# Kernel optimization log

Measured on AMD Instinct MI355X. Metric: run time of the kernel, lower is better.

## Reference

```python
import jax, jax.numpy as jnp
import numpy as np

NEG_SLOPE = 0.01  # torch nn.LeakyReLU default


def setup_inputs() -> dict:
    key = jax.random.key(0)
    k1, k2 = jax.random.split(key)
    B, L, N = 32, 512, 1024
    X = jax.random.normal(k1, (B, L, N), dtype=jnp.float32)
    W = jax.random.normal(k2, (1, 2 * L), dtype=jnp.float32) * (1.0 / np.sqrt(2 * L))
    return {"X": X, "W": W}


def reference(X, W):
    # X: [B, L, N]; W: [1, 2L] weight of Linear(2L, 1, bias=False)
    L = X.shape[1]
    N = X.shape[2]
    w1 = W[0, :L]   # applied to X[:, :, i]
    w2 = W[0, L:]   # applied to X[:, :, j]
    s1 = jnp.einsum('bln,l->bn', X, w1)  # [B, N]
    s2 = jnp.einsum('bln,l->bn', X, w2)  # [B, N]
    # e[b,i,j] = leaky_relu(s1[b,i] + s2[b,j]) for i != j, 0 on the diagonal
    e = jax.nn.leaky_relu(s1[:, :, None] + s2[:, None, :], NEG_SLOPE)  # [B, N, N]
    diag = jnp.eye(N, dtype=bool)
    e = jnp.where(diag[None, :, :], 0.0, e)
    # softmax over dim=1 (over i), matching torch.softmax(e, dim=1)
    alpha = jax.nn.softmax(e, axis=1)  # [B, N, N]
    # h = bmm(alpha, X^T)^T: h[b,l,i] = sum_j alpha[b,i,j] * X[b,l,j]
    h = jnp.einsum('bij,blj->bli', alpha, X)  # [B, L, N]
    return jax.nn.sigmoid(h)
```

## Files before the change

kernel.cpp:

```cpp
#include <hip/hip_runtime.h>
#include <hip/hip_bf16.h>

#define BATCH 32
#define LSEQ  512
#define NDIM  1024
#define NSPLIT 16

typedef __attribute__((ext_vector_type(8))) short bf16x8;
typedef __attribute__((ext_vector_type(4))) float f32x4;

__device__ __forceinline__ unsigned short f2bf(float x) {
    __hip_bfloat16 h = __float2bfloat16(x);
    return __builtin_bit_cast(unsigned short, h);
}

__global__ __launch_bounds__(256) void prep_kernel(
    const float* __restrict__ X, const float* __restrict__ W,
    unsigned short* __restrict__ Xb, float* __restrict__ P1, float* __restrict__ P2)
{
    __shared__ float sw[2 * LSEQ];
    int tid = threadIdx.x;
    for (int i = tid; i < 2 * LSEQ; i += 256) sw[i] = W[i];
    __syncthreads();

    int b  = blockIdx.y;
    int sp = blockIdx.x;
    int l0 = sp * (LSEQ / NSPLIT);
    size_t base = ((size_t)b * LSEQ + l0) * NDIM + tid * 4;
    const float* xp = X + base;
    unsigned short* xbp = Xb + base;

    float a0=0,a1=0,a2=0,a3=0, c0=0,c1=0,c2=0,c3=0;
    for (int l = 0; l < LSEQ / NSPLIT; ++l) {
        float4 x = *(const float4*)(xp + (size_t)l * NDIM);
        float w1 = sw[l0 + l], w2 = sw[LSEQ + l0 + l];
        a0 = fmaf(x.x, w1, a0); a1 = fmaf(x.y, w1, a1);
        a2 = fmaf(x.z, w1, a2); a3 = fmaf(x.w, w1, a3);
        c0 = fmaf(x.x, w2, c0); c1 = fmaf(x.y, w2, c1);
        c2 = fmaf(x.z, w2, c2); c3 = fmaf(x.w, w2, c3);
        ushort4 u; u.x = f2bf(x.x); u.y = f2bf(x.y); u.z = f2bf(x.z); u.w = f2bf(x.w);
        *(ushort4*)(xbp + (size_t)l * NDIM) = u;
    }
    size_t po = ((size_t)sp * BATCH + b) * NDIM + tid * 4;
    *(float4*)(P1 + po) = make_float4(a0, a1, a2, a3);
    *(float4*)(P2 + po) = make_float4(c0, c1, c2, c3);
}

__global__ __launch_bounds__(256) void stats_kernel(
    const float* __restrict__ P1, const float* __restrict__ P2,
    float* __restrict__ s1, float* __restrict__ s2, float* __restrict__ rd)
{
    __shared__ float s1s[NDIM];
    __shared__ float s2s[128];
    int t = threadIdx.x;
    int b = blockIdx.x >> 3, sl = blockIdx.x & 7;
    int j0 = sl * 128;

    #pragma unroll
    for (int q = 0; q < 4; ++q) {
        int n = q * 256 + t;
        float a = 0.f;
        #pragma unroll
        for (int sp = 0; sp < NSPLIT; ++sp)
            a += P1[((size_t)sp * BATCH + b) * NDIM + n];
        s1s[n] = a;
        if (sl == 0) s1[b * NDIM + n] = a;
    }
    if (t < 128) {
        int j = j0 + t;
        float c = 0.f;
        #pragma unroll
        for (int sp = 0; sp < NSPLIT; ++sp)
            c += P2[((size_t)sp * BATCH + b) * NDIM + j];
        s2s[t] = c;
        s2[b * NDIM + j] = c;
    }
    __syncthreads();

    int jl = t >> 1, half = t & 1;
    int jg = j0 + jl;
    float s2j = s2s[jl];
    float sum = 0.f;
    int i0 = half * 512;
    for (int i = i0; i < i0 + 512; ++i) {
        float v = s1s[i] + s2j;
        v = fmaxf(v, 0.01f * v);
        if (i == jg) v = 0.f;
        sum += __expf(v);
    }
    sum += __shfl_xor(sum, 1);
    if (half == 0) rd[b * NDIM + jg] = 1.0f / sum;
}

__global__ __launch_bounds__(256) void btgen_kernel(
    const float* __restrict__ s1, const float* __restrict__ s2,
    const float* __restrict__ rd, unsigned short* __restrict__ Bt)
{
    int wid = threadIdx.x >> 6, lane = threadIdx.x & 63;
    int r = blockIdx.x * 4 + wid;
    int b = r >> 10, i = r & 1023;
    float s1i = s1[r];
    const float* s2b = s2 + b * NDIM;
    const float* rdb = rd + b * NDIM;
    unsigned short* outp = Bt + (size_t)r * NDIM;

    #pragma unroll
    for (int q = 0; q < 2; ++q) {
        int j0 = q * 512 + lane * 8;
        float sv[8], rv[8];
        #pragma unroll
        for (int h = 0; h < 2; ++h) {
            float4 s4 = *(const float4*)(s2b + j0 + h * 4);
            float4 r4 = *(const float4*)(rdb + j0 + h * 4);
            sv[h*4+0]=s4.x; sv[h*4+1]=s4.y; sv[h*4+2]=s4.z; sv[h*4+3]=s4.w;
            rv[h*4+0]=r4.x; rv[h*4+1]=r4.y; rv[h*4+2]=r4.z; rv[h*4+3]=r4.w;
        }
        bf16x8 v;
        #pragma unroll
        for (int k = 0; k < 8; ++k) {
            float e = s1i + sv[k];
            e = fmaxf(e, 0.01f * e);
            if (j0 + k == i) e = 0.f;
            v[k] = (short)f2bf(__expf(e) * rv[k]);
        }
        *(bf16x8*)&outp[j0] = v;
    }
}

__global__ __launch_bounds__(256) void gemm_kernel(
    const unsigned short* __restrict__ Xb, const unsigned short* __restrict__ Bt,
    float* __restrict__ out)
{
    __shared__ __align__(16) unsigned short Xs[2 * 128 * 32];
    __shared__ __align__(16) unsigned short Bs[2 * 128 * 32];

    int tid = threadIdx.x, wid = tid >> 6, lane = tid & 63;
    int wm = wid >> 1, wn = wid & 1;

    int flat = blockIdx.x;
    int xcd   = flat & 7;
    int idx   = flat >> 3;
    int bg    = idx >> 5;
    int inner = idx & 31;
    int b  = bg * 8 + xcd;
    int n0 = (inner & 7) * 128;
    int l0 = (inner >> 3) * 128;

    const unsigned short* Xg = Xb + ((size_t)b * LSEQ + l0) * NDIM;
    const unsigned short* Bg = Bt + ((size_t)b * NDIM + n0) * NDIM;

    int rin = lane >> 2, ch = lane & 3;

    f32x4 acc[4][4] = {};

    for (int kb = 0; kb < 16; ++kb) {
        int k0 = kb * 64;
        __syncthreads();
        #pragma unroll
        for (int kh = 0; kh < 2; ++kh) {
            #pragma unroll
            for (int q = 0; q < 2; ++q) {
                int row = wid * 32 + q * 16 + rin;
                int kg = k0 + kh * 32 + ch * 8;
                const unsigned short* gx = Xg + (size_t)row * NDIM + kg;
                const unsigned short* gb = Bg + (size_t)row * NDIM + kg;
                unsigned short* lx = &Xs[kh * 4096 + (wid * 32 + q * 16) * 32];
                unsigned short* lb = &Bs[kh * 4096 + (wid * 32 + q * 16) * 32];
                __builtin_amdgcn_global_load_lds(
                    (const __attribute__((address_space(1))) void*)gx,
                    (__attribute__((address_space(3))) void*)lx, 16, 0, 0);
                __builtin_amdgcn_global_load_lds(
                    (const __attribute__((address_space(1))) void*)gb,
                    (__attribute__((address_space(3))) void*)lb, 16, 0, 0);
            }
        }
        __syncthreads();

        int rsel = lane & 15, ksel = (lane >> 4) * 8;
        #pragma unroll
        for (int kh = 0; kh < 2; ++kh) {
            bf16x8 av[4], bv[4];
            #pragma unroll
            for (int mi = 0; mi < 4; ++mi)
                av[mi] = *(const bf16x8*)&Xs[kh * 4096 + (wm * 64 + mi * 16 + rsel) * 32 + ksel];
            #pragma unroll
            for (int ni = 0; ni < 4; ++ni)
                bv[ni] = *(const bf16x8*)&Bs[kh * 4096 + (wn * 64 + ni * 16 + rsel) * 32 + ksel];
            #pragma unroll
            for (int mi = 0; mi < 4; ++mi)
                #pragma unroll
                for (int ni = 0; ni < 4; ++ni)
                    acc[mi][ni] = __builtin_amdgcn_mfma_f32_16x16x32_bf16(
                        av[mi], bv[ni], acc[mi][ni], 0, 0, 0);
        }
    }

    float* outb = out + ((size_t)b * LSEQ + l0) * NDIM + n0;
    int rq = lane >> 4, cl = lane & 15;
    #pragma unroll
    for (int mi = 0; mi < 4; ++mi)
        #pragma unroll
        for (int ni = 0; ni < 4; ++ni) {
            int col = wn * 64 + ni * 16 + cl;
            #pragma unroll
            for (int r2 = 0; r2 < 4; ++r2) {
                int row = wm * 64 + mi * 16 + rq * 4 + r2;
                float v = acc[mi][ni][r2];
                outb[(size_t)row * NDIM + col] = 1.0f / (1.0f + __expf(-v));
            }
        }
}

extern "C" void kernel_launch(void* const* d_in, const int* in_sizes, int n_in,
                              void* d_out, int out_size, void* d_ws, size_t ws_size,
                              hipStream_t stream) {
    (void)in_sizes; (void)n_in; (void)out_size; (void)ws_size;
    const float* X = (const float*)d_in[0];
    const float* W = (const float*)d_in[1];
    float* out = (float*)d_out;

    float* s1 = (float*)d_ws;
    float* s2 = s1 + BATCH * NDIM;
    float* rd = s2 + BATCH * NDIM;
    float* P1 = rd + BATCH * NDIM;
    float* P2 = P1 + (size_t)NSPLIT * BATCH * NDIM;
    unsigned short* Xb = (unsigned short*)(P2 + (size_t)NSPLIT * BATCH * NDIM);
    unsigned short* Bt = Xb + (size_t)BATCH * LSEQ * NDIM;

    prep_kernel<<<dim3(NSPLIT, BATCH), 256, 0, stream>>>(X, W, Xb, P1, P2);
    stats_kernel<<<256, 256, 0, stream>>>(P1, P2, s1, s2, rd);
    btgen_kernel<<<(BATCH * NDIM) / 4, 256, 0, stream>>>(s1, s2, rd, Bt);
    gemm_kernel<<<1024, 256, 0, stream>>>(Xb, Bt, out);
}
```

Measured before the change: 199.6 us.

## Rewrite GEMM with 256x256 tiles, 4-stage LDS pipeline and swizzled layout

The batched GEMM kernel now uses 512-thread blocks computing 256x256 output tiles, fed by a 4-deep ring of LDS buffers filled with direct global-to-LDS loads and gated by vmcnt waits with one barrier per k-step. LDS rows are XOR-swizzled to avoid bank conflicts, and MFMA issue is wrapped in setprio. The aim is to hide global-load latency and raise data reuse per loaded byte. In exchange each wave holds more accumulators and the block uses 128KB of LDS, and only 256 blocks are launched, which may limit occupancy and load balance across CUs.

```diff
diff --git a/kernel.cpp b/kernel.cpp
--- a/kernel.cpp
+++ b/kernel.cpp
@@ -127,89 +127,111 @@
     }
 }
 
-__global__ __launch_bounds__(256) void gemm_kernel(
+#define WAITVM(n) asm volatile("s_waitcnt vmcnt(" #n ")" ::: "memory")
+#define FENCE()   asm volatile("" ::: "memory")
+
+#define DO_STAGE(bufi) {                                                        \
+    _Pragma("unroll")                                                           \
+    for (int j = 0; j < 4; ++j) {                                               \
+        __builtin_amdgcn_global_load_lds(                                       \
+            (const __attribute__((address_space(1))) void*)srcp[j],             \
+            (__attribute__((address_space(3))) void*)(LdsC + (bufi) * 32768 +   \
+                                                      ldst0 + j * 8192),        \
+            16, 0, 0);                                                          \
+        srcp[j] += 64;                       \
+    } }
+
+#define COMPUTE(bufi) {                                                         \
+    const char* Lb = LdsC + (bufi) * 32768;                                     \
+    bf16x8 av[8]; bf16x8 bv[4];                                                 \
+    _Pragma("unroll")                                                           \
+    for (int mi = 0; mi < 8; ++mi)                                              \
+        av[mi] = *(const bf16x8*)(Lb + abase0 + mi * 2048);                     \
+    _Pragma("unroll")                                                           \
+    for (int ni = 0; ni < 4; ++ni)                                              \
+        bv[ni] = *(const bf16x8*)(Lb + bbase0 + ni * 2048);                     \
+    __builtin_amdgcn_s_setprio(1);                                              \
+    _Pragma("unroll")                                                           \
+    for (int ni = 0; ni < 4; ++ni)                                              \
+        _Pragma("unroll")                                                       \
+        for (int mi = 0; mi < 8; ++mi)                                          \
+            acc[mi][ni] = __builtin_amdgcn_mfma_f32_16x16x32_bf16(              \
+                av[mi], bv[ni], acc[mi][ni], 0, 0, 0);                          \
+    __builtin_amdgcn_s_setprio(0);                                              \
+}
+
+__global__ __launch_bounds__(512, 2) void gemm_kernel(
     const unsigned short* __restrict__ Xb, const unsigned short* __restrict__ Bt,
     float* __restrict__ out)
 {
-    __shared__ __align__(16) unsigned short Xs[2 * 128 * 32];
-    __shared__ __align__(16) unsigned short Bs[2 * 128 * 32];
-
-    int tid = threadIdx.x, wid = tid >> 6, lane = tid & 63;
-    int wm = wid >> 1, wn = wid & 1;
-
-    int flat = blockIdx.x;
+    __shared__ __align__(16) unsigned short LDSU[65536];
+    char* LdsC = (char*)LDSU;
+
+    const int tid = threadIdx.x, lane = tid & 63, wid = tid >> 6;
+    const int wm = wid >> 2, wn = wid & 3;
+
+    int flat  = blockIdx.x;
     int xcd   = flat & 7;
-    int idx   = flat >> 3;
-    int bg    = idx >> 5;
-    int inner = idx & 31;
-    int b  = bg * 8 + xcd;
-    int n0 = (inner & 7) * 128;
-    int l0 = (inner >> 3) * 128;
-
-    const unsigned short* Xg = Xb + ((size_t)b * LSEQ + l0) * NDIM;
-    const unsigned short* Bg = Bt + ((size_t)b * NDIM + n0) * NDIM;
-
-    int rin = lane >> 2, ch = lane & 3;
-
-    f32x4 acc[4][4] = {};
-
-    for (int kb = 0; kb < 16; ++kb) {
-        int k0 = kb * 64;
-        __syncthreads();
-        #pragma unroll
-        for (int kh = 0; kh < 2; ++kh) {
-            #pragma unroll
-            for (int q = 0; q < 2; ++q) {
-                int row = wid * 32 + q * 16 + rin;
-                int kg = k0 + kh * 32 + ch * 8;
-                const unsigned short* gx = Xg + (size_t)row * NDIM + kg;
-                const unsigned short* gb = Bg + (size_t)row * NDIM + kg;
-                unsigned short* lx = &Xs[kh * 4096 + (wid * 32 + q * 16) * 32];
-                unsigned short* lb = &Bs[kh * 4096 + (wid * 32 + q * 16) * 32];
-                __builtin_amdgcn_global_load_lds(
-                    (const __attribute__((address_space(1))) void*)gx,
-                    (__attribute__((address_space(3))) void*)lx, 16, 0, 0);
-                __builtin_amdgcn_global_load_lds(
-                    (const __attribute__((address_space(1))) void*)gb,
-                    (__attribute__((address_space(3))) void*)lb, 16, 0, 0);
-            }
-        }
-        __syncthreads();
-
-        int rsel = lane & 15, ksel = (lane >> 4) * 8;
-        #pragma unroll
-        for (int kh = 0; kh < 2; ++kh) {
-            bf16x8 av[4], bv[4];
-            #pragma unroll
-            for (int mi = 0; mi < 4; ++mi)
-                av[mi] = *(const bf16x8*)&Xs[kh * 4096 + (wm * 64 + mi * 16 + rsel) * 32 + ksel];
-            #pragma unroll
-            for (int ni = 0; ni < 4; ++ni)
-                bv[ni] = *(const bf16x8*)&Bs[kh * 4096 + (wn * 64 + ni * 16 + rsel) * 32 + ksel];
-            #pragma unroll
-            for (int mi = 0; mi < 4; ++mi)
-                #pragma unroll
-                for (int ni = 0; ni < 4; ++ni)
-                    acc[mi][ni] = __builtin_amdgcn_mfma_f32_16x16x32_bf16(
-                        av[mi], bv[ni], acc[mi][ni], 0, 0, 0);
-        }
-    }
+    int p     = flat >> 3;
+    int b     = (p >> 3) * 8 + xcd;
+    int inner = p & 7;
+    int mt = inner & 1, nt = inner >> 1;
+    int l0 = mt * 256, n0 = nt * 256;
+
+    const char* XgB = (const char*)(Xb + ((size_t)b * LSEQ + l0) * NDIM);
+    const char* BgB = (const char*)(Bt + ((size_t)b * NDIM + n0) * NDIM);
+
+    const char* srcp[4];
+    #pragma unroll
+    for (int j = 0; j < 4; ++j) {
+        int c = tid + j * 512;
+        int r = c >> 3, slot = c & 7;
+        int off = (slot * 16) ^ ((r & 7) << 4);
+        srcp[j] = (off < 64) ? XgB + (size_t)r * 2048 + off
+                             : BgB + (size_t)r * 2048 + (off - 64);
+    }
+    const int ldst0 = wid * 1024;
+
+    const int rsel = lane & 15, kq = lane >> 4;
+    const int swz  = (rsel & 7) << 4;
+    const int abase0 = wm * 16384 + rsel * 128 + ((kq * 16) ^ swz);
+    const int bbase0 = wn * 8192  + rsel * 128 + (((64 + kq * 16)) ^ swz);
+
+    f32x4 acc[8][4] = {};
+
+    DO_STAGE(0); DO_STAGE(1); DO_STAGE(2);
+
+    for (int t = 0; t < 29; ++t) {
+        WAITVM(8);
+        __builtin_amdgcn_s_barrier();
+        FENCE();
+        DO_STAGE((t + 3) & 3);
+        COMPUTE(t & 3);
+    }
+    WAITVM(8); __builtin_amdgcn_s_barrier(); FENCE(); COMPUTE(1);
+    WAITVM(4); __builtin_amdgcn_s_barrier(); FENCE(); COMPUTE(2);
+    WAITVM(0); __builtin_amdgcn_s_barrier(); FENCE(); COMPUTE(3);
 
     float* outb = out + ((size_t)b * LSEQ + l0) * NDIM + n0;
-    int rq = lane >> 4, cl = lane & 15;
-    #pragma unroll
-    for (int mi = 0; mi < 4; ++mi)
+    const int rq = lane >> 4, cl = lane & 15;
+    #pragma unroll
+    for (int mi = 0; mi < 8; ++mi)
         #pragma unroll
         for (int ni = 0; ni < 4; ++ni) {
             int col = wn * 64 + ni * 16 + cl;
             #pragma unroll
             for (int r2 = 0; r2 < 4; ++r2) {
-                int row = wm * 64 + mi * 16 + rq * 4 + r2;
+                int row = wm * 128 + mi * 16 + rq * 4 + r2;
                 float v = acc[mi][ni][r2];
                 outb[(size_t)row * NDIM + col] = 1.0f / (1.0f + __expf(-v));
             }
         }
 }
+
+#undef WAITVM
+#undef FENCE
+#undef DO_STAGE
+#undef COMPUTE
 
 extern "C" void kernel_launch(void* const* d_in, const int* in_sizes, int n_in,
                               void* d_out, int out_size, void* d_ws, size_t ws_size,
@@ -230,5 +252,5 @@
     prep_kernel<<<dim3(NSPLIT, BATCH), 256, 0, stream>>>(X, W, Xb, P1, P2);
     stats_kernel<<<256, 256, 0, stream>>>(P1, P2, s1, s2, rd);
     btgen_kernel<<<(BATCH * NDIM) / 4, 256, 0, stream>>>(s1, s2, rd, Bt);
-    gemm_kernel<<<1024, 256, 0, stream>>>(Xb, Bt, out);
-}
+    gemm_kernel<<<256, 512, 0, stream>>>(Xb, Bt, out);
+}
```

After: 183.7 us. 8.0% less time.
